# Performance work log

Measured on AMD Instinct MI355X. Metric: run time of the kernel, lower is better.

The kernel has to match this reference:

```python
import jax, jax.numpy as jnp
import numpy as np

B, T, D_MODEL = 2, 1024, 1024
H, DEPTH = 8, 5
DH = D_MODEL // H


def setup_inputs() -> dict:
    key = jax.random.key(0)
    k_x, k_wp, k_bp, k_wv, k_wo = jax.random.split(key, 5)
    x = jax.random.normal(k_x, (B, T, D_MODEL), dtype=jnp.float32)
    # Parameters stored as [in, out] (y = x @ W + b), equivalent math to nn.Linear.
    Wp = jax.random.normal(k_wp, (D_MODEL, H * DEPTH), dtype=jnp.float32) * 0.02
    bp = jnp.zeros((H * DEPTH,), dtype=jnp.float32)
    Wv = jax.random.normal(k_wv, (D_MODEL, D_MODEL), dtype=jnp.float32) * 0.02
    Wo = jax.random.normal(k_wo, (D_MODEL, D_MODEL), dtype=jnp.float32) * 0.02
    return {"x": x, "Wp": Wp, "bp": bp, "Wv": Wv, "Wo": Wo}


def reference(x, Wp, bp, Wv, Wo):
    Bx, Tx, d = x.shape
    # soft binary path decisions: B,H,T,DEPTH
    paths = jax.nn.sigmoid(x @ Wp + bp)              # B,T,H*DEPTH
    paths = paths.reshape(Bx, Tx, H, DEPTH).transpose(0, 2, 1, 3)  # B,H,T,DEPTH
    # pairwise per-level agreement: B,H,Tq,Tk,DEPTH
    pq = paths[:, :, :, None, :]
    pk = paths[:, :, None, :, :]
    agree = pq * pk + (1.0 - pq) * (1.0 - pk)
    # shared-prefix length via cumprod over depth, summed
    sim = jnp.cumprod(agree, axis=-1).sum(axis=-1) / DEPTH  # B,H,Tq,Tk
    # causal mask
    mask = jnp.triu(jnp.ones((Tx, Tx), dtype=bool), k=1)
    sim = jnp.where(mask[None, None], -jnp.inf, sim)
    attn = jax.nn.softmax(sim, axis=-1)              # B,H,T,T
    V = (x @ Wv).reshape(Bx, Tx, H, DH).transpose(0, 2, 1, 3)  # B,H,T,dh
    ctx = jnp.einsum('bhqk,bhkd->bhqd', attn, V)
    ctx = ctx.transpose(0, 2, 1, 3).reshape(Bx, Tx, d)
    return ctx @ Wo
```

## Files before the change

kernel.cpp:

```cpp
#include <hip/hip_runtime.h>
#include <hip/hip_bf16.h>

#define B_ 2
#define T_ 1024
#define D_ 1024
#define H_ 8
#define DEPTH_ 5
#define DH_ 128

typedef short s16x8 __attribute__((ext_vector_type(8)));
typedef short s16x4 __attribute__((ext_vector_type(4)));
typedef float f32x4 __attribute__((ext_vector_type(4)));

__device__ inline short f2bf(float f) {
  __hip_bfloat16 h = __float2bfloat16(f);
  return *reinterpret_cast<short*>(&h);
}

#define MFMA16(a, b, c) __builtin_amdgcn_mfma_f32_16x16x32_bf16(a, b, c, 0, 0, 0)

typedef __attribute__((address_space(3))) unsigned int lds_u32_t;
typedef __attribute__((address_space(1))) unsigned int glb_u32_t;
__device__ __forceinline__ void glds16(const void* g, void* l) {
  __builtin_amdgcn_global_load_lds((const glb_u32_t*)g, (lds_u32_t*)l, 16, 0,
                                   0);
}

#define BARRIER()                     \
  {                                   \
    asm volatile("" ::: "memory");    \
    __builtin_amdgcn_s_barrier();     \
    asm volatile("" ::: "memory");    \
  }

__global__ __launch_bounds__(256) void prep_kernel(
    const float* __restrict__ Wv, const float* __restrict__ Wo,
    const float* __restrict__ Wp, const float* __restrict__ x,
    short* __restrict__ WBt, short* __restrict__ Wot,
    short* __restrict__ xb) {
  int tid = threadIdx.x;
  if (blockIdx.z < 2) {
    const float* W = blockIdx.z ? Wo : Wv;
    short* Wt = blockIdx.z ? Wot : WBt;
    __shared__ float tile[64][65];
    int k0 = blockIdx.y * 64, n0 = blockIdx.x * 64;
#pragma unroll
    for (int i = 0; i < 4; ++i) {
      int idx = tid + i * 256;
      int r = idx >> 4, c4 = (idx & 15) * 4;
      float4 v = *(const float4*)&W[(size_t)(k0 + r) * D_ + n0 + c4];
      tile[r][c4 + 0] = v.x;
      tile[r][c4 + 1] = v.y;
      tile[r][c4 + 2] = v.z;
      tile[r][c4 + 3] = v.w;
    }
    __syncthreads();
#pragma unroll
    for (int j = 0; j < 2; ++j) {
      int idx = tid + j * 256;
      int n = idx >> 3, k8 = (idx & 7) * 8;
      s16x8 outv;
#pragma unroll
      for (int jj = 0; jj < 8; ++jj) outv[jj] = f2bf(tile[k8 + jj][n]);
      *(s16x8*)&Wt[(size_t)(n0 + n) * D_ + k0 + k8] = outv;
    }
  } else {
    int bid = blockIdx.y * 16 + blockIdx.x;
#pragma unroll
    for (int c = 0; c < 4; ++c) {
      size_t idx = (size_t)bid * 8192 + c * 2048 + tid * 8;
      float4 f0 = *(const float4*)&x[idx];
      float4 f1 = *(const float4*)&x[idx + 4];
      s16x8 v;
      v[0] = f2bf(f0.x); v[1] = f2bf(f0.y);
      v[2] = f2bf(f0.z); v[3] = f2bf(f0.w);
      v[4] = f2bf(f1.x); v[5] = f2bf(f1.y);
      v[6] = f2bf(f1.z); v[7] = f2bf(f1.w);
      *(s16x8*)&xb[idx] = v;
    }
    if (bid < 4) {
#pragma unroll
      for (int it = 0; it < 8; ++it) {
        int item = bid * 2048 + it * 256 + tid;
        int row = item >> 7, k8 = (item & 127) * 8;
        s16x8 v;
        if (row < H_ * DEPTH_) {
#pragma unroll
          for (int j = 0; j < 8; ++j)
            v[j] = f2bf(Wp[(size_t)(k8 + j) * (H_ * DEPTH_) + row]);
        } else {
#pragma unroll
          for (int j = 0; j < 8; ++j) v[j] = 0;
        }
        *(s16x8*)&WBt[(size_t)(1024 + row) * D_ + k8] = v;
      }
    }
  }
}

template <int MODE>
__global__ __launch_bounds__(256) void gemm128(
    const short* __restrict__ A, const short* __restrict__ Bt,
    float* __restrict__ Cf, short* __restrict__ Vt,
    const float* __restrict__ bp, float* __restrict__ paths_t) {
  __shared__ short As[2][128 * 64];
  __shared__ short Bs[2][64 * 64];
  const int K = D_;
  int tid = threadIdx.x;
  int bm = blockIdx.y << 7, bn = blockIdx.x << 6;
  int w = tid >> 6, lane = tid & 63;
  int wm = (w >> 1) * 64, wn = (w & 1) * 32;
  int g = lane >> 4, fr = lane & 15;
  f32x4 acc[4][2] = {};

  int r8 = lane >> 3;
  int scg = (lane & 7) ^ r8;
  const short* Asrc[4];
  const short* Bsrc[2];
#pragma unroll
  for (int i = 0; i < 4; ++i)
    Asrc[i] = A + (size_t)(bm + w * 32 + i * 8 + r8) * K + scg * 8;
#pragma unroll
  for (int i = 0; i < 2; ++i)
    Bsrc[i] = Bt + (size_t)(bn + w * 16 + i * 8 + r8) * K + scg * 8;

#define STAGE(BUF, K0)                                    \
  {                                                       \
    glds16(Asrc[0] + (K0), &As[BUF][(w * 32 + 0) * 64]);  \
    glds16(Asrc[1] + (K0), &As[BUF][(w * 32 + 8) * 64]);  \
    glds16(Asrc[2] + (K0), &As[BUF][(w * 32 + 16) * 64]); \
    glds16(Asrc[3] + (K0), &As[BUF][(w * 32 + 24) * 64]); \
    glds16(Bsrc[0] + (K0), &Bs[BUF][(w * 16 + 0) * 64]);  \
    glds16(Bsrc[1] + (K0), &Bs[BUF][(w * 16 + 8) * 64]);  \
  }

#define COMPUTE(BUF)                                                   \
  {                                                                    \
    _Pragma("unroll") for (int ks = 0; ks < 2; ++ks) {                 \
      int slot = ((ks * 4 + g) ^ (fr & 7)) * 8;                        \
      s16x8 a0 = *(const s16x8*)&As[BUF][(wm + fr) * 64 + slot];       \
      s16x8 a1 = *(const s16x8*)&As[BUF][(wm + 16 + fr) * 64 + slot];  \
      s16x8 a2 = *(const s16x8*)&As[BUF][(wm + 32 + fr) * 64 + slot];  \
      s16x8 a3 = *(const s16x8*)&As[BUF][(wm + 48 + fr) * 64 + slot];  \
      s16x8 b0 = *(const s16x8*)&Bs[BUF][(wn + fr) * 64 + slot];       \
      s16x8 b1 = *(const s16x8*)&Bs[BUF][(wn + 16 + fr) * 64 + slot];  \
      acc[0][0] = MFMA16(a0, b0, acc[0][0]);                           \
      acc[0][1] = MFMA16(a0, b1, acc[0][1]);                           \
      acc[1][0] = MFMA16(a1, b0, acc[1][0]);                           \
      acc[1][1] = MFMA16(a1, b1, acc[1][1]);                           \
      acc[2][0] = MFMA16(a2, b0, acc[2][0]);                           \
      acc[2][1] = MFMA16(a2, b1, acc[2][1]);                           \
      acc[3][0] = MFMA16(a3, b0, acc[3][0]);                           \
      acc[3][1] = MFMA16(a3, b1, acc[3][1]);                           \
    }                                                                  \
  }

  const int NKT = K / 64;
  STAGE(0, 0);
  for (int kt = 0; kt < NKT; kt += 2) {
    BARRIER();
    if (kt + 1 < NKT) {
      STAGE(1, (kt + 1) * 64);
      asm volatile("s_waitcnt vmcnt(6)" ::: "memory");
    } else {
      asm volatile("s_waitcnt vmcnt(0)" ::: "memory");
    }
    BARRIER();
    COMPUTE(0);
    BARRIER();
    if (kt + 2 < NKT) {
      STAGE(0, (kt + 2) * 64);
      asm volatile("s_waitcnt vmcnt(6)" ::: "memory");
    } else {
      asm volatile("s_waitcnt vmcnt(0)" ::: "memory");
    }
    BARRIER();
    COMPUTE(1);
  }
#undef STAGE
#undef COMPUTE

  int col = lane & 15, rbase = (lane >> 4) * 4;
  if (MODE == 0) {
#pragma unroll
    for (int mi = 0; mi < 4; ++mi)
#pragma unroll
      for (int ni = 0; ni < 2; ++ni)
#pragma unroll
        for (int r = 0; r < 4; ++r)
          Cf[(size_t)(bm + wm + mi * 16 + rbase + r) * D_ + bn + wn +
             ni * 16 + col] = acc[mi][ni][r];
  } else if (bn < 1024) {
#pragma unroll
    for (int mi = 0; mi < 4; ++mi)
#pragma unroll
      for (int ni = 0; ni < 2; ++ni) {
        int m = bm + wm + mi * 16 + rbase;
        int n = bn + wn + ni * 16 + col;
        int b = m >> 10, t = m & (T_ - 1);
        int h = n >> 7, dh = n & (DH_ - 1);
        s16x4 v4;
#pragma unroll
        for (int r = 0; r < 4; ++r) v4[r] = f2bf(acc[mi][ni][r]);
        *(s16x4*)&Vt[((size_t)((b * H_ + h) * DH_ + dh)) * T_ + t] = v4;
      }
  } else {
#pragma unroll
    for (int ni = 0; ni < 2; ++ni) {
      int pn = wn + ni * 16 + col;
      if (pn < H_ * DEPTH_) {
        float bias = bp[pn];
        int h = pn / DEPTH_, d = pn % DEPTH_;
#pragma unroll
        for (int mi = 0; mi < 4; ++mi)
#pragma unroll
          for (int r = 0; r < 4; ++r) {
            int m = bm + wm + mi * 16 + rbase + r;
            int b = m >> 10, t = m & (T_ - 1);
            float pv = 1.f / (1.f + __expf(-(acc[mi][ni][r] + bias)));
            paths_t[(((size_t)(b * H_ + h) * T_ + t) * DEPTH_) + d] = pv;
          }
      }
    }
  }
}

#define LS2 136

__global__ __launch_bounds__(512) void attn_kernel(
    const float* __restrict__ paths_t, const short* __restrict__ Vt,
    short* __restrict__ ctxb) {
  int bh = blockIdx.y;
  int b = bh >> 3, h = bh & 7;
  int bx = blockIdx.x;
  int w = threadIdx.x >> 6, lane = threadIdx.x & 63;
  int g = lane >> 4, fr = lane & 15;

  __shared__ short Vs[DH_ * 128];
  __shared__ short Ss[32 * LS2];
  __shared__ float lsum_s[32];

  const float* pb = paths_t + (size_t)bh * T_ * DEPTH_;
  const short* vb = Vt + (size_t)bh * DH_ * T_;

  int r4 = lane >> 4, cg = lane & 15;
  const short* Vsrc[4];
  short* Vdst[4];
#pragma unroll
  for (int i = 0; i < 4; ++i) {
    int row = w * 16 + i * 4 + r4;
    int scol = (cg ^ (row & 15)) * 8;
    Vsrc[i] = vb + (size_t)row * T_ + scol;
    Vdst[i] = &Vs[(w * 16 + i * 4) * 128];
  }

  for (int half = 0; half < 2; ++half) {
    int qt = half ? (31 - bx) : bx;
    int q0 = qt * 32;
    int nkt = (qt >> 2) + 1;

    float pq[4][DEPTH_], mq[4][DEPTH_];
#pragma unroll
    for (int j = 0; j < 4; ++j) {
      const float* qr = pb + (size_t)(q0 + w * 4 + j) * DEPTH_;
#pragma unroll
      for (int d = 0; d < DEPTH_; ++d) {
        pq[j][d] = qr[d];
        mq[j][d] = 1.f - pq[j][d];
      }
    }
    f32x4 acc[2] = {{0.f, 0.f, 0.f, 0.f}, {0.f, 0.f, 0.f, 0.f}};
    float part[4] = {};

    for (int kt = 0; kt < nkt; ++kt) {
      int k0 = kt * 128;
      __syncthreads();
      int kA = k0 + lane, kB = k0 + 64 + lane;
      const float* krA = pb + (size_t)kA * DEPTH_;
      const float* krB = pb + (size_t)kB * DEPTH_;
      float pkA[DEPTH_], mkA[DEPTH_], pkB[DEPTH_], mkB[DEPTH_];
#pragma unroll
      for (int d = 0; d < DEPTH_; ++d) {
        pkA[d] = krA[d];
        pkB[d] = krB[d];
      }
#pragma unroll
      for (int i = 0; i < 4; ++i) glds16(Vsrc[i] + k0, Vdst[i]);
#pragma unroll
      for (int d = 0; d < DEPTH_; ++d) {
        mkA[d] = 1.f - pkA[d];
        mkB[d] = 1.f - pkB[d];
      }
#pragma unroll
      for (int j = 0; j < 4; ++j) {
        int qg = q0 + w * 4 + j;
        {
          float a0 = fmaf(pq[j][0], pkA[0], mq[j][0] * mkA[0]);
          float a1 = fmaf(pq[j][1], pkA[1], mq[j][1] * mkA[1]);
          float a2 = fmaf(pq[j][2], pkA[2], mq[j][2] * mkA[2]);
          float a3 = fmaf(pq[j][3], pkA[3], mq[j][3] * mkA[3]);
          float a4 = fmaf(pq[j][4], pkA[4], mq[j][4] * mkA[4]);
          float t4 = 1.f + a4;
          float t3 = fmaf(a3, t4, 1.f);
          float t2 = fmaf(a2, t3, 1.f);
          float t1 = fmaf(a1, t2, 1.f);
          float s = a0 * t1;
          float wv = (kA <= qg) ? __expf(s * 0.2f) : 0.f;
          part[j] += wv;
          Ss[(w * 4 + j) * LS2 + lane] = f2bf(wv);
        }
        {
          float a0 = fmaf(pq[j][0], pkB[0], mq[j][0] * mkB[0]);
          float a1 = fmaf(pq[j][1], pkB[1], mq[j][1] * mkB[1]);
          float a2 = fmaf(pq[j][2], pkB[2], mq[j][2] * mkB[2]);
          float a3 = fmaf(pq[j][3], pkB[3], mq[j][3] * mkB[3]);
          float a4 = fmaf(pq[j][4], pkB[4], mq[j][4] * mkB[4]);
          float t4 = 1.f + a4;
          float t3 = fmaf(a3, t4, 1.f);
          float t2 = fmaf(a2, t3, 1.f);
          float t1 = fmaf(a1, t2, 1.f);
          float s = a0 * t1;
          float wv = (kB <= qg) ? __expf(s * 0.2f) : 0.f;
          part[j] += wv;
          Ss[(w * 4 + j) * LS2 + 64 + lane] = f2bf(wv);
        }
      }
      __syncthreads();
#pragma unroll
      for (int ks = 0; ks < 4; ++ks) {
        int ko = ks * 32 + g * 8;
        int sl = ((ks * 4 + g) ^ fr) * 8;
        s16x8 sa0 = *(const s16x8*)&Ss[fr * LS2 + ko];
        s16x8 sa1 = *(const s16x8*)&Ss[(16 + fr) * LS2 + ko];
        s16x8 vv = *(const s16x8*)&Vs[(w * 16 + fr) * 128 + sl];
        acc[0] = MFMA16(sa0, vv, acc[0]);
        acc[1] = MFMA16(sa1, vv, acc[1]);
      }
    }
#pragma unroll
    for (int j = 0; j < 4; ++j) {
      float s = part[j];
#pragma unroll
      for (int off = 32; off >= 1; off >>= 1) s += __shfl_xor(s, off, 64);
      if (lane == j) lsum_s[w * 4 + j] = s;
    }
    __syncthreads();
    int col = fr, rbase = g * 4;
#pragma unroll
    for (int qt2 = 0; qt2 < 2; ++qt2)
#pragma unroll
      for (int r = 0; r < 4; ++r) {
        int ql = qt2 * 16 + rbase + r;
        int dh = w * 16 + col;
        float val = acc[qt2][r] / lsum_s[ql];
        ctxb[(size_t)(b * T_ + q0 + ql) * D_ + h * DH_ + dh] = f2bf(val);
      }
    __syncthreads();
  }
}

extern "C" void kernel_launch(void* const* d_in, const int* in_sizes, int n_in,
                              void* d_out, int out_size, void* d_ws,
                              size_t ws_size, hipStream_t stream) {
  const float* x = (const float*)d_in[0];
  const float* Wp = (const float*)d_in[1];
  const float* bp = (const float*)d_in[2];
  const float* Wv = (const float*)d_in[3];
  const float* Wo = (const float*)d_in[4];
  float* out = (float*)d_out;

  char* ws = (char*)d_ws;
  float* paths_t = (float*)ws;
  short* Vt = (short*)(ws + 327680);
  short* WBt = (short*)(ws + 4521984);
  short* Wot = (short*)(ws + 6750208);
  short* ctxb = (short*)(ws + 8847360);
  short* xb = (short*)(ws + 13041664);

  prep_kernel<<<dim3(16, 16, 3), 256, 0, stream>>>(Wv, Wo, Wp, x, WBt, Wot,
                                                   xb);
  gemm128<1><<<dim3(17, 16), 256, 0, stream>>>(xb, WBt, nullptr, Vt, bp,
                                               paths_t);
  attn_kernel<<<dim3(16, B_ * H_), 512, 0, stream>>>(paths_t, Vt, ctxb);
  gemm128<0><<<dim3(16, 16), 256, 0, stream>>>(ctxb, Wot, out, nullptr,
                                               nullptr, nullptr);
}
```

Measured before the change: 132.2 us.

## Triple-buffer GEMM K-loop and swizzle 1D grid block mapping

New measurement: 130.0 us. No clear change (-1.6%).

```diff
diff --git a/kernel.cpp b/kernel.cpp
--- a/kernel.cpp
+++ b/kernel.cpp
@@ -103,11 +103,17 @@
     const short* __restrict__ A, const short* __restrict__ Bt,
     float* __restrict__ Cf, short* __restrict__ Vt,
     const float* __restrict__ bp, float* __restrict__ paths_t) {
-  __shared__ short As[2][128 * 64];
-  __shared__ short Bs[2][64 * 64];
+  __shared__ short As[3][128 * 64];
+  __shared__ short Bs[3][64 * 64];
   const int K = D_;
   int tid = threadIdx.x;
-  int bm = blockIdx.y << 7, bn = blockIdx.x << 6;
+
+  int lin = blockIdx.x;
+  int cpx = gridDim.x >> 3;
+  int swz = (lin & 7) * cpx + (lin >> 3);
+  const int GM = 16;
+  int bm = (swz % GM) << 7, bn = (swz / GM) << 6;
+
   int w = tid >> 6, lane = tid & 63;
   int wm = (w >> 1) * 64, wn = (w & 1) * 32;
   int g = lane >> 4, fr = lane & 15;
@@ -155,28 +161,33 @@
     }                                                                  \
   }
 
-  const int NKT = K / 64;
   STAGE(0, 0);
-  for (int kt = 0; kt < NKT; kt += 2) {
-    BARRIER();
-    if (kt + 1 < NKT) {
-      STAGE(1, (kt + 1) * 64);
+  STAGE(1, 64);
+  for (int b = 0; b < 15; b += 3) {
+    BARRIER();
+    STAGE(2, (b + 2) * 64);
+    asm volatile("s_waitcnt vmcnt(12)" ::: "memory");
+    BARRIER();
+    COMPUTE(0);
+    BARRIER();
+    STAGE(0, (b + 3) * 64);
+    asm volatile("s_waitcnt vmcnt(12)" ::: "memory");
+    BARRIER();
+    COMPUTE(1);
+    BARRIER();
+    if (b < 12) {
+      STAGE(1, (b + 4) * 64);
+      asm volatile("s_waitcnt vmcnt(12)" ::: "memory");
+    } else {
       asm volatile("s_waitcnt vmcnt(6)" ::: "memory");
-    } else {
-      asm volatile("s_waitcnt vmcnt(0)" ::: "memory");
-    }
-    BARRIER();
-    COMPUTE(0);
-    BARRIER();
-    if (kt + 2 < NKT) {
-      STAGE(0, (kt + 2) * 64);
-      asm volatile("s_waitcnt vmcnt(6)" ::: "memory");
-    } else {
-      asm volatile("s_waitcnt vmcnt(0)" ::: "memory");
-    }
-    BARRIER();
-    COMPUTE(1);
-  }
+    }
+    BARRIER();
+    COMPUTE(2);
+  }
+  BARRIER();
+  asm volatile("s_waitcnt vmcnt(0)" ::: "memory");
+  BARRIER();
+  COMPUTE(0);
 #undef STAGE
 #undef COMPUTE
 
@@ -379,9 +390,9 @@
 
   prep_kernel<<<dim3(16, 16, 3), 256, 0, stream>>>(Wv, Wo, Wp, x, WBt, Wot,
                                                    xb);
-  gemm128<1><<<dim3(17, 16), 256, 0, stream>>>(xb, WBt, nullptr, Vt, bp,
-                                               paths_t);
+  gemm128<1><<<dim3(17 * 16), 256, 0, stream>>>(xb, WBt, nullptr, Vt, bp,
+                                                paths_t);
   attn_kernel<<<dim3(16, B_ * H_), 512, 0, stream>>>(paths_t, Vt, ctxb);
-  gemm128<0><<<dim3(16, 16), 256, 0, stream>>>(ctxb, Wot, out, nullptr,
-                                               nullptr, nullptr);
-}
+  gemm128<0><<<dim3(16 * 16), 256, 0, stream>>>(ctxb, Wot, out, nullptr,
+                                                nullptr, nullptr);
+}
```
